# Kernel optimization log

Hardware: AMD Instinct MI355X
Metric: run time of the kernel (lower is better)

The kernel has to match this reference:

```python
import jax, jax.numpy as jnp
import numpy as np

N_NODES = 100000
N_EDGES = 1600000
N_FEAT = 64
HID = 64
HL = 256
N_GRAPHS = 512


def _lin(k, i, o):
    return (jax.random.normal(k, (i, o), jnp.float32) / np.sqrt(i)).astype(jnp.float32)


def setup_inputs() -> dict:
    key = jax.random.key(0)
    ks = jax.random.split(key, 20)
    inp = {
        "x": jax.random.normal(ks[0], (N_NODES, N_FEAT), jnp.float32),
        "edge_index": jax.random.randint(ks[1], (2, N_EDGES), 0, N_NODES),
        "batch": jnp.sort(jax.random.randint(ks[2], (N_NODES,), 0, N_GRAPHS)),
        "T": jax.random.normal(ks[3], (N_GRAPHS, 1), jnp.float32),
    }
    dims = [(N_FEAT, HID), (HID, HID), (HID, HID), (HID, HID)]
    for i, (di, do) in enumerate(dims):
        inp[f"wrel{i}"] = _lin(ks[4 + 3 * i], di, do)
        inp[f"brel{i}"] = jnp.zeros((do,), jnp.float32)
        inp[f"wroot{i}"] = _lin(ks[5 + 3 * i], di, do)
    inp["w1"] = _lin(ks[16], 3 * HID + 1, HL)
    inp["b1"] = jnp.zeros((HL,), jnp.float32)
    inp["w2"] = _lin(ks[17], HL, HL)
    inp["b2"] = jnp.zeros((HL,), jnp.float32)
    inp["w3"] = _lin(ks[18], HL, 1)
    inp["b3"] = jnp.zeros((1,), jnp.float32)
    return inp


def reference(x, edge_index, batch, T,
              wrel0, brel0, wroot0,
              wrel1, brel1, wroot1,
              wrel2, brel2, wroot2,
              wrel3, brel3, wroot3,
              w1, b1, w2, b2, w3, b3):
    src, dst = edge_index[0], edge_index[1]

    def conv(h, wr, br, wq):
        # PyG GraphConv: W_root h_i + W_rel * sum_{j->i} h_j + b_rel
        agg = jax.ops.segment_sum(h[src], dst, num_segments=N_NODES)
        return agg @ wr + br + h @ wq

    h = jax.nn.relu(conv(x, wrel0, brel0, wroot0))
    h = jax.nn.relu(conv(h, wrel1, brel1, wroot1))
    h = jax.nn.relu(conv(h, wrel2, brel2, wroot2))
    h = conv(h, wrel3, brel3, wroot3)  # no relu on conv2 (matches original)

    # global add / mean / max pools over graph ids
    s = jax.ops.segment_sum(h, batch, num_segments=N_GRAPHS)
    cnt = jax.ops.segment_sum(jnp.ones((N_NODES, 1), h.dtype), batch, num_segments=N_GRAPHS)
    mean = s / jnp.maximum(cnt, 1.0)
    mx = jax.ops.segment_max(h, batch, num_segments=N_GRAPHS)
    mx = jnp.where(jnp.isfinite(mx), mx, 0.0)  # empty segments -> 0

    out = jnp.concatenate([mx, mean, s, T], axis=1)  # [G, 3*HID+1]
    o = jax.nn.relu(out @ w1 + b1)
    o = jax.nn.relu(o @ w2 + b2)  # dropout is identity in eval mode
    return o @ w3 + b3
```

## Files before the change

kernel.cpp:

```cpp
#include <hip/hip_runtime.h>
#include <hip/hip_bf16.h>
#include <math.h>

#define N_NODES 100000
#define N_EDGES 1600000
#define N_FEAT 64
#define HID 64
#define HL 256
#define N_GRAPHS 512

#define BUCKET_BITS 7
#define BUCKET_SIZE 128
#define NB ((N_NODES + BUCKET_SIZE - 1) / BUCKET_SIZE)
#define LOFS_W (NB + 1)
#define CAP 3584
#define LREC_CAP 3584
#define EDGES_PER_BLOCK 4096
#define SCAT_BLOCKS ((N_EDGES + EDGES_PER_BLOCK - 1) / EDGES_PER_BLOCK)
#define F2B_BLOCKS (N_NODES * 16 / 256)
#define WPREP_BLOCKS 128
#define ZOFF ((unsigned int)N_NODES * 128u)

typedef short vbf8 __attribute__((ext_vector_type(8)));
typedef float vf4 __attribute__((ext_vector_type(4)));
typedef float vf2 __attribute__((ext_vector_type(2)));

__device__ __forceinline__ unsigned short f2b(float f) {
    unsigned int u = __float_as_uint(f);
    return (unsigned short)((u + 0x7FFFu + ((u >> 16) & 1u)) >> 16);
}
__device__ __forceinline__ float b2f(unsigned short u) {
    return __uint_as_float(((unsigned int)u) << 16);
}
__device__ __forceinline__ unsigned pk2(float lo, float hi) {
    float2 f; f.x = lo; f.y = hi;
    __hip_bfloat162 h = __float22bfloat162_rn(f);
    unsigned r;
    __builtin_memcpy(&r, &h, 4);
    return r;
}
__device__ __forceinline__ vf2 bpair(unsigned int d) {
    vf2 r;
    r.x = __uint_as_float(d << 16);
    r.y = __uint_as_float(d & 0xFFFF0000u);
    return r;
}


__global__ __launch_bounds__(256) void k_mega(
        const int* __restrict__ src, const int* __restrict__ dst,
        int* __restrict__ lofs, unsigned int* __restrict__ ebuf,
        const float4* __restrict__ x, uint2* __restrict__ xb,
        const float* __restrict__ wroot0, const float* __restrict__ wrel0,
        const float* __restrict__ wroot1, const float* __restrict__ wrel1,
        const float* __restrict__ wroot2, const float* __restrict__ wrel2,
        const float* __restrict__ wroot3, const float* __restrict__ wrel3,
        unsigned short* __restrict__ wt) {
    __shared__ int lh[NB];
    __shared__ int lsc[256];
    __shared__ unsigned lrec[EDGES_PER_BLOCK];
    int bid = blockIdx.x;
    int t = threadIdx.x;

    if (bid < SCAT_BLOCKS) {
        for (int i = t; i < NB; i += 256) lh[i] = 0;
        __syncthreads();
        int i0 = bid * EDGES_PER_BLOCK;
        int i1 = min(N_EDGES, i0 + EDGES_PER_BLOCK);
        int cnt = i1 - i0;
        for (int i = i0 + t; i < i1; i += 256)
            atomicAdd(&lh[dst[i] >> BUCKET_BITS], 1);
        __syncthreads();
        int v[4];
        int s = 0;
        int base4 = t * 4;
#pragma unroll
        for (int j = 0; j < 4; j++) {
            v[j] = (base4 + j < NB) ? lh[base4 + j] : 0;
            s += v[j];
        }
        lsc[t] = s;
        __syncthreads();
        for (int off = 1; off < 256; off <<= 1) {
            int xx = lsc[t];
            int y = (t >= off) ? lsc[t - off] : 0;
            __syncthreads();
            lsc[t] = xx + y;
            __syncthreads();
        }
        int run = lsc[t] - s;
        int* lrow = lofs + (size_t)bid * LOFS_W;
#pragma unroll
        for (int j = 0; j < 4; j++) {
            int b = base4 + j;
            if (b < NB) {
                lrow[b] = run;
                lh[b] = run;
            }
            run += v[j];
        }
        if (t == 255) lrow[NB] = cnt;
        __syncthreads();
        for (int i = i0 + t; i < i1; i += 256) {
            int sN = src[i], d = dst[i];
            int b = d >> BUCKET_BITS;
            int p = atomicAdd(&lh[b], 1);
            lrec[p] = ((unsigned)sN << 7) | (unsigned)(d & 127);
        }
        __syncthreads();
        unsigned* eb = ebuf + (size_t)bid * EDGES_PER_BLOCK;
        for (int j = t; j < cnt; j += 256) eb[j] = lrec[j];
    } else if (bid < SCAT_BLOCKS + F2B_BLOCKS) {
        int i = (bid - SCAT_BLOCKS) * 256 + t;
        if (i < N_NODES * 16) {
            float4 v = x[i];
            uint2 o;
            o.x = pk2(v.x, v.y);
            o.y = pk2(v.z, v.w);
            xb[i] = o;
        }
    } else {
        int gi = (bid - SCAT_BLOCKS - F2B_BLOCKS) * 256 + t;
        if (gi < 4 * 64 * 128) {
            int layer = gi >> 13;
            int i = gi & 8191;
            int nn = i >> 7, k = i & 127;
            const float* wr = (layer == 0) ? wroot0 : (layer == 1) ? wroot1
                             : (layer == 2) ? wroot2 : wroot3;
            const float* wl = (layer == 0) ? wrel0 : (layer == 1) ? wrel1
                             : (layer == 2) ? wrel2 : wrel3;
            float v = (k < 64) ? wr[k * 64 + nn] : wl[(k - 64) * 64 + nn];
            wt[gi] = f2b(v);
        }
    }
}


__global__ __launch_bounds__(256) void k_fscatter2(
        const unsigned int* __restrict__ ebuf, const int* __restrict__ lofs,
        int2* __restrict__ re, unsigned int* __restrict__ soff,
        unsigned short* __restrict__ hbA, unsigned short* __restrict__ hbB, int n) {
    __shared__ int rcnt[512];
    __shared__ int rbase[512];
    __shared__ int rpre[512];
    __shared__ int tsc[256];
    __shared__ unsigned lrec[LREC_CAP];
    __shared__ int lcnt[BUCKET_SIZE];
    __shared__ int sc[BUCKET_SIZE];
    __shared__ int cur[BUCKET_SIZE];
    int b = blockIdx.x;
    int n0 = b * BUCKET_SIZE;
    int t = threadIdx.x;
    if (b == 0 && t < 16) {
        uint4 z = make_uint4(0u, 0u, 0u, 0u);
        unsigned short* hp = (t < 8) ? hbA : hbB;
        ((uint4*)(hp + (size_t)N_NODES * 64))[t & 7] = z;
    }
    for (int blk = t; blk < 512; blk += 256) {
        int c = 0, ba = 0;
        if (blk < SCAT_BLOCKS) {
            const int* lr = lofs + (size_t)blk * LOFS_W + b;
            ba = lr[0];
            c = lr[1] - ba;
        }
        rcnt[blk] = c;
        rbase[blk] = ba;
    }
    __syncthreads();
    int c0 = rcnt[2 * t], c1 = rcnt[2 * t + 1];
    tsc[t] = c0 + c1;
    __syncthreads();
    for (int off = 1; off < 256; off <<= 1) {
        int xx = tsc[t];
        int y = (t >= off) ? tsc[t - off] : 0;
        __syncthreads();
        tsc[t] = xx + y;
        __syncthreads();
    }
    int ex = tsc[t] - (c0 + c1);
    rpre[2 * t] = ex;
    rpre[2 * t + 1] = ex + c0;
    __syncthreads();
    int cb = tsc[255];
    for (int blk = t; blk < SCAT_BLOCKS; blk += 256) {
        int c = rcnt[blk];
        int dsto = rpre[blk];
        const unsigned* sp = ebuf + (size_t)blk * EDGES_PER_BLOCK + rbase[blk];
        for (int j = 0; j < c; j++) lrec[dsto + j] = sp[j];
    }
    if (t < BUCKET_SIZE) lcnt[t] = 0;
    __syncthreads();
    for (int r = t; r < cb; r += 256)
        atomicAdd(&lcnt[lrec[r] & 127u], 1);
    __syncthreads();
    int v = 0, pcnt = 0;
    if (t < BUCKET_SIZE) {
        v = lcnt[t];
        pcnt = (v + 7) & ~7;
        sc[t] = pcnt;
    }
    __syncthreads();
    for (int off = 1; off < BUCKET_SIZE; off <<= 1) {
        int xx = 0;
        if (t < BUCKET_SIZE) {
            xx = sc[t];
            if (t >= off) xx += sc[t - off];
        }
        __syncthreads();
        if (t < BUCKET_SIZE) sc[t] = xx;
        __syncthreads();
    }
    if (t < BUCKET_SIZE) {
        int start = b * CAP + sc[t] - pcnt;
        if (n0 + t < n) re[n0 + t] = make_int2(start, start + v);
        cur[t] = start;
        for (int z = start + v; z < start + pcnt; z++) soff[z] = ZOFF;
    }
    __syncthreads();
    for (int r = t; r < cb; r += 256) {
        unsigned rec = lrec[r];
        int p = atomicAdd(&cur[rec & 127u], 1);
        soff[p] = rec & ~127u;
    }
}


__global__ __launch_bounds__(256) void k_agg(
    const unsigned short* __restrict__ hb, unsigned short* __restrict__ aggb,
    const int2* __restrict__ re, const unsigned int* __restrict__ soff, int n) {
    int lane = threadIdx.x & 63;
    int i = (blockIdx.x * 256 + threadIdx.x) >> 6;
    if (i >= n) return;
    int q = lane >> 3;
    int sl = lane & 7;
    int2 bounds = re[i];
    int e0 = bounds.x, e1 = bounds.y;
    int iters = (e1 - e0 + 7) >> 3;
    const char* base = (const char*)hb + sl * 16;

    vf2 A[4], B[4];
#pragma unroll
    for (int f = 0; f < 4; f++) { A[f] = (vf2){0.f, 0.f}; B[f] = (vf2){0.f, 0.f}; }

    int eq = e0 + q;
    int it = 0;
    for (; it + 2 <= iters; it += 2) {
        int ea = eq + it * 8, eb = ea + 8;
        unsigned oa = __builtin_nontemporal_load(soff + ea);
        unsigned ob = __builtin_nontemporal_load(soff + eb);
        uint4 da = *(const uint4*)(base + oa);
        uint4 db = *(const uint4*)(base + ob);
        A[0] += bpair(da.x); A[1] += bpair(da.y);
        A[2] += bpair(da.z); A[3] += bpair(da.w);
        B[0] += bpair(db.x); B[1] += bpair(db.y);
        B[2] += bpair(db.z); B[3] += bpair(db.w);
    }
    if (it < iters) {
        int ea = eq + it * 8;
        unsigned oa = __builtin_nontemporal_load(soff + ea);
        uint4 da = *(const uint4*)(base + oa);
        A[0] += bpair(da.x); A[1] += bpair(da.y);
        A[2] += bpair(da.z); A[3] += bpair(da.w);
    }

    float f[8];
#pragma unroll
    for (int k = 0; k < 4; k++) {
        vf2 s2 = A[k] + B[k];
        float slo = s2.x, shi = s2.y;
        slo += __shfl_xor(slo, 8);
        slo += __shfl_xor(slo, 16);
        slo += __shfl_xor(slo, 32);
        shi += __shfl_xor(shi, 8);
        shi += __shfl_xor(shi, 16);
        shi += __shfl_xor(shi, 32);
        f[2 * k] = slo;
        f[2 * k + 1] = shi;
    }
    if (q == 0) {
        uint4 o;
        o.x = pk2(f[0], f[1]);
        o.y = pk2(f[2], f[3]);
        o.z = pk2(f[4], f[5]);
        o.w = pk2(f[6], f[7]);
        *(uint4*)((char*)aggb + (size_t)i * 128 + sl * 16) = o;
    }
}


template <int RELU>
__global__ __launch_bounds__(256) void k_gemm(
    const unsigned short* __restrict__ hb, const unsigned short* __restrict__ aggb,
    const unsigned short* __restrict__ wt, const float* __restrict__ brel,
    unsigned short* __restrict__ hbout, int n) {
    __shared__ float sc[4][16 * 68];

    int tid = threadIdx.x;
    int w = tid >> 6, l = tid & 63;
    int lm = l & 15, q = l >> 4;
    int r0 = blockIdx.x * 64 + w * 16;

    int arow = r0 + lm;
    if (arow >= n) arow = n - 1;
    const unsigned short* ah = hb + (size_t)arow * 64 + q * 8;
    const unsigned short* aa = aggb + (size_t)arow * 64 + q * 8;
    vbf8 afr[4];
    afr[0] = *(const vbf8*)(ah);
    afr[1] = *(const vbf8*)(ah + 32);
    afr[2] = *(const vbf8*)(aa);
    afr[3] = *(const vbf8*)(aa + 32);

    vf4 acc[4];
#pragma unroll
    for (int t = 0; t < 4; t++) acc[t] = (vf4){0.f, 0.f, 0.f, 0.f};

#pragma unroll
    for (int t = 0; t < 4; t++) {
        const unsigned short* wrow = wt + (size_t)(t * 16 + lm) * 128 + q * 8;
#pragma unroll
        for (int s = 0; s < 4; s++) {
            vbf8 bfr = *(const vbf8*)(wrow + s * 32);
            acc[t] = __builtin_amdgcn_mfma_f32_16x16x32_bf16(afr[s], bfr, acc[t], 0, 0, 0);
        }
    }

    float* sw_ = sc[w];
#pragma unroll
    for (int t = 0; t < 4; t++) {
        float b = brel[t * 16 + lm];
#pragma unroll
        for (int i = 0; i < 4; i++) {
            float v = acc[t][i] + b;
            if (RELU) v = fmaxf(v, 0.f);
            sw_[(q * 4 + i) * 68 + t * 16 + lm] = v;
        }
    }
    int rr = l >> 2, cs = l & 3;
    int node = r0 + rr;
    if (node < n) {
        const float* rp = sw_ + rr * 68 + cs * 16;
        float4 v0 = *(const float4*)(rp);
        float4 v1 = *(const float4*)(rp + 4);
        float4 v2 = *(const float4*)(rp + 8);
        float4 v3 = *(const float4*)(rp + 12);
        uint4 o0, o1;
        o0.x = pk2(v0.x, v0.y);
        o0.y = pk2(v0.z, v0.w);
        o0.z = pk2(v1.x, v1.y);
        o0.w = pk2(v1.z, v1.w);
        o1.x = pk2(v2.x, v2.y);
        o1.y = pk2(v2.z, v2.w);
        o1.z = pk2(v3.x, v3.y);
        o1.w = pk2(v3.z, v3.w);
        uint4* op = (uint4*)(hbout + (size_t)node * 64 + cs * 16);
        op[0] = o0;
        op[1] = o1;
    }
}


__global__ __launch_bounds__(256) void k_poolmlp(
    const unsigned short* __restrict__ hb, const int* __restrict__ batch,
    const float* __restrict__ T, const float* __restrict__ w1,
    const float* __restrict__ b1, const float* __restrict__ w2,
    const float* __restrict__ b2, const float* __restrict__ w3,
    const float* __restrict__ b3, float* __restrict__ out, int n) {
    __shared__ float psum[4][64];
    __shared__ float pmax[4][64];
    __shared__ float sin_[200];
    __shared__ float so1[256];
    __shared__ float red[256];
    int g = blockIdx.x, t = threadIdx.x;
    int l = t & 63, c = t >> 6;

    int lo = 0, hi = n;
    while (lo < hi) { int m = (lo + hi) >> 1; if (batch[m] < g) lo = m + 1; else hi = m; }
    int s0 = lo;
    int lo2 = s0, hi2 = n;
    while (lo2 < hi2) { int m = (lo2 + hi2) >> 1; if (batch[m] < g + 1) lo2 = m + 1; else hi2 = m; }
    int s1 = lo2;

    float sa0 = 0.f, sa1 = 0.f, sa2 = 0.f, sa3 = 0.f;
    float ma0 = -INFINITY, ma1 = -INFINITY, ma2 = -INFINITY, ma3 = -INFINITY;
    int nn = s0 + c;
    for (; nn + 12 < s1; nn += 16) {
        float v0 = b2f(hb[(size_t)nn * 64 + l]);
        float v1 = b2f(hb[(size_t)(nn + 4) * 64 + l]);
        float v2 = b2f(hb[(size_t)(nn + 8) * 64 + l]);
        float v3 = b2f(hb[(size_t)(nn + 12) * 64 + l]);
        sa0 += v0; sa1 += v1; sa2 += v2; sa3 += v3;
        ma0 = fmaxf(ma0, v0); ma1 = fmaxf(ma1, v1);
        ma2 = fmaxf(ma2, v2); ma3 = fmaxf(ma3, v3);
    }
    for (; nn < s1; nn += 4) {
        float v = b2f(hb[(size_t)nn * 64 + l]);
        sa0 += v;
        ma0 = fmaxf(ma0, v);
    }
    psum[c][l] = (sa0 + sa1) + (sa2 + sa3);
    pmax[c][l] = fmaxf(fmaxf(ma0, ma1), fmaxf(ma2, ma3));
    __syncthreads();
    if (t < 64) {
        float s = (psum[0][t] + psum[1][t]) + (psum[2][t] + psum[3][t]);
        float mx = fmaxf(fmaxf(pmax[0][t], pmax[1][t]), fmaxf(pmax[2][t], pmax[3][t]));
        int cnt = s1 - s0;
        float mean = s / fmaxf((float)cnt, 1.f);
        if (cnt == 0) mx = 0.f;
        sin_[t] = mx;
        sin_[64 + t] = mean;
        sin_[128 + t] = s;
        if (t == 0) {
            sin_[192] = T[g];
#pragma unroll
            for (int z = 193; z < 200; z++) sin_[z] = 0.f;
        }
    }
    __syncthreads();

    float a = b1[t];
    {
        float wv[8];
        for (int k = 0; k < 192; k += 8) {
#pragma unroll
            for (int u = 0; u < 8; u++) wv[u] = w1[(k + u) * 256 + t];
#pragma unroll
            for (int u = 0; u < 8; u++) a += sin_[k + u] * wv[u];
        }
        a += sin_[192] * w1[192 * 256 + t];
    }
    a = fmaxf(a, 0.f);
    so1[t] = a;
    __syncthreads();

    float a2 = b2[t];
    {
        float wv[8];
        for (int k = 0; k < 256; k += 8) {
#pragma unroll
            for (int u = 0; u < 8; u++) wv[u] = w2[(k + u) * 256 + t];
#pragma unroll
            for (int u = 0; u < 8; u++) a2 += so1[k + u] * wv[u];
        }
    }
    a2 = fmaxf(a2, 0.f);
    red[t] = a2 * w3[t];
    __syncthreads();
    for (int s = 128; s > 0; s >>= 1) {
        if (t < s) red[t] += red[t + s];
        __syncthreads();
    }
    if (t == 0) out[g] = red[0] + b3[0];
}

extern "C" void kernel_launch(void* const* d_in, const int* in_sizes, int n_in,
                              void* d_out, int out_size, void* d_ws, size_t ws_size,
                              hipStream_t stream) {
    const int N = N_NODES, E = N_EDGES, G = N_GRAPHS;

    const float* x = (const float*)d_in[0];
    const int* ei = (const int*)d_in[1];
    const int* batch = (const int*)d_in[2];
    const float* T = (const float*)d_in[3];
    const float* wrel[4] = {(const float*)d_in[4], (const float*)d_in[7],
                            (const float*)d_in[10], (const float*)d_in[13]};
    const float* brel[4] = {(const float*)d_in[5], (const float*)d_in[8],
                            (const float*)d_in[11], (const float*)d_in[14]};
    const float* wroot[4] = {(const float*)d_in[6], (const float*)d_in[9],
                             (const float*)d_in[12], (const float*)d_in[15]};
    const float* w1 = (const float*)d_in[16];
    const float* b1 = (const float*)d_in[17];
    const float* w2 = (const float*)d_in[18];
    const float* b2 = (const float*)d_in[19];
    const float* w3 = (const float*)d_in[20];
    const float* b3 = (const float*)d_in[21];
    float* out = (float*)d_out;

    const int* esrc = ei;
    const int* edst = ei + E;

    char* ws = (char*)d_ws;
    size_t off = 0;
    auto alloc = [&](size_t bytes) {
        size_t r = off;
        off = (off + bytes + 255) & ~(size_t)255;
        return r;
    };
    int* lofs = (int*)(ws + alloc((size_t)SCAT_BLOCKS * LOFS_W * 4));
    int2* re = (int2*)(ws + alloc((size_t)N * 8));
    unsigned int* soff = (unsigned int*)(ws + alloc((size_t)NB * CAP * 4));
    unsigned int* ebuf = (unsigned int*)(ws + alloc((size_t)SCAT_BLOCKS * EDGES_PER_BLOCK * 4));
    unsigned short* hbA = (unsigned short*)(ws + alloc((size_t)N * 64 * 2 + 128));
    unsigned short* hbB = (unsigned short*)(ws + alloc((size_t)N * 64 * 2 + 128));
    unsigned short* aggb = (unsigned short*)(ws + alloc((size_t)N * 64 * 2));
    unsigned short* wt = (unsigned short*)(ws + alloc((size_t)4 * 64 * 128 * 2));

    k_mega<<<SCAT_BLOCKS + F2B_BLOCKS + WPREP_BLOCKS, 256, 0, stream>>>(
        esrc, edst, lofs, ebuf, (const float4*)x, (uint2*)hbA,
        wroot[0], wrel[0], wroot[1], wrel[1],
        wroot[2], wrel[2], wroot[3], wrel[3], wt);
    k_fscatter2<<<NB, 256, 0, stream>>>(ebuf, lofs, re, soff, hbA, hbB, N);

    int agg_blocks = (N * 64 + 255) / 256;
    int gemm_blocks = (N + 63) / 64;

    k_agg<<<agg_blocks, 256, 0, stream>>>(hbA, aggb, re, soff, N);
    k_gemm<1><<<gemm_blocks, 256, 0, stream>>>(hbA, aggb, wt + 0 * 8192, brel[0], hbB, N);

    k_agg<<<agg_blocks, 256, 0, stream>>>(hbB, aggb, re, soff, N);
    k_gemm<1><<<gemm_blocks, 256, 0, stream>>>(hbB, aggb, wt + 1 * 8192, brel[1], hbA, N);

    k_agg<<<agg_blocks, 256, 0, stream>>>(hbA, aggb, re, soff, N);
    k_gemm<1><<<gemm_blocks, 256, 0, stream>>>(hbA, aggb, wt + 2 * 8192, brel[2], hbB, N);

    k_agg<<<agg_blocks, 256, 0, stream>>>(hbB, aggb, re, soff, N);
    k_gemm<0><<<gemm_blocks, 256, 0, stream>>>(hbB, aggb, wt + 3 * 8192, brel[3], hbA, N);

    k_poolmlp<<<G, 256, 0, stream>>>(hbA, batch, T, w1, b1, w2, b2, w3, b3, out, N);
}
```

Measured before the change: 398.4 us.

## Map eight nodes per wavefront in aggregation instead of one node per wave

The aggregation kernel now gives each 8-lane group its own destination node, so a wavefront handles 8 nodes instead of splitting one node's edges across 8 lane groups. This drops the cross-lane shuffle reduction and cuts the block count by 8x. Each group walks its own padded edge list, with the loop bound set to the maximum count in the wave, and out-of-range slots point at a zero row. The cost is divergence from uneven degrees within a wave, plus serial per-node latency chains of four gathers per iteration.

```diff
diff --git a/kernel.cpp b/kernel.cpp
--- a/kernel.cpp
+++ b/kernel.cpp
@@ -229,60 +229,60 @@
     const unsigned short* __restrict__ hb, unsigned short* __restrict__ aggb,
     const int2* __restrict__ re, const unsigned int* __restrict__ soff, int n) {
     int lane = threadIdx.x & 63;
-    int i = (blockIdx.x * 256 + threadIdx.x) >> 6;
-    if (i >= n) return;
-    int q = lane >> 3;
+    int wv = (blockIdx.x * 256 + threadIdx.x) >> 6;
+    int m = lane >> 3;
     int sl = lane & 7;
-    int2 bounds = re[i];
-    int e0 = bounds.x, e1 = bounds.y;
-    int iters = (e1 - e0 + 7) >> 3;
+    int i = wv * 8 + m;
+    if (wv * 8 >= n) return;
+    int ii = min(i, n - 1);
+    int2 bd = re[ii];
+    int e0 = bd.x;
+    int pc = (i < n) ? ((bd.y - bd.x + 7) & ~7) : 0;
+
+    int mx = pc;
+    mx = max(mx, __shfl_xor(mx, 8));
+    mx = max(mx, __shfl_xor(mx, 16));
+    mx = max(mx, __shfl_xor(mx, 32));
+
     const char* base = (const char*)hb + sl * 16;
-
     vf2 A[4], B[4];
 #pragma unroll
     for (int f = 0; f < 4; f++) { A[f] = (vf2){0.f, 0.f}; B[f] = (vf2){0.f, 0.f}; }
 
-    int eq = e0 + q;
-    int it = 0;
-    for (; it + 2 <= iters; it += 2) {
-        int ea = eq + it * 8, eb = ea + 8;
-        unsigned oa = __builtin_nontemporal_load(soff + ea);
-        unsigned ob = __builtin_nontemporal_load(soff + eb);
-        uint4 da = *(const uint4*)(base + oa);
-        uint4 db = *(const uint4*)(base + ob);
-        A[0] += bpair(da.x); A[1] += bpair(da.y);
-        A[2] += bpair(da.z); A[3] += bpair(da.w);
-        B[0] += bpair(db.x); B[1] += bpair(db.y);
-        B[2] += bpair(db.z); B[3] += bpair(db.w);
-    }
-    if (it < iters) {
-        int ea = eq + it * 8;
-        unsigned oa = __builtin_nontemporal_load(soff + ea);
-        uint4 da = *(const uint4*)(base + oa);
-        A[0] += bpair(da.x); A[1] += bpair(da.y);
-        A[2] += bpair(da.z); A[3] += bpair(da.w);
-    }
-
-    float f[8];
-#pragma unroll
-    for (int k = 0; k < 4; k++) {
-        vf2 s2 = A[k] + B[k];
-        float slo = s2.x, shi = s2.y;
-        slo += __shfl_xor(slo, 8);
-        slo += __shfl_xor(slo, 16);
-        slo += __shfl_xor(slo, 32);
-        shi += __shfl_xor(shi, 8);
-        shi += __shfl_xor(shi, 16);
-        shi += __shfl_xor(shi, 32);
-        f[2 * k] = slo;
-        f[2 * k + 1] = shi;
-    }
-    if (q == 0) {
+    for (int it = 0; it < mx; it += 4) {
+        int t0 = it, t1 = it + 1, t2 = it + 2, t3 = it + 3;
+        unsigned o0 = __builtin_nontemporal_load(soff + e0 + ((t0 < pc) ? t0 : 0));
+        unsigned o1 = __builtin_nontemporal_load(soff + e0 + ((t1 < pc) ? t1 : 0));
+        unsigned o2 = __builtin_nontemporal_load(soff + e0 + ((t2 < pc) ? t2 : 0));
+        unsigned o3 = __builtin_nontemporal_load(soff + e0 + ((t3 < pc) ? t3 : 0));
+        o0 = (t0 < pc) ? o0 : ZOFF;
+        o1 = (t1 < pc) ? o1 : ZOFF;
+        o2 = (t2 < pc) ? o2 : ZOFF;
+        o3 = (t3 < pc) ? o3 : ZOFF;
+        uint4 d0 = *(const uint4*)(base + o0);
+        uint4 d1 = *(const uint4*)(base + o1);
+        uint4 d2 = *(const uint4*)(base + o2);
+        uint4 d3 = *(const uint4*)(base + o3);
+        A[0] += bpair(d0.x); A[1] += bpair(d0.y);
+        A[2] += bpair(d0.z); A[3] += bpair(d0.w);
+        B[0] += bpair(d1.x); B[1] += bpair(d1.y);
+        B[2] += bpair(d1.z); B[3] += bpair(d1.w);
+        A[0] += bpair(d2.x); A[1] += bpair(d2.y);
+        A[2] += bpair(d2.z); A[3] += bpair(d2.w);
+        B[0] += bpair(d3.x); B[1] += bpair(d3.y);
+        B[2] += bpair(d3.z); B[3] += bpair(d3.w);
+    }
+
+    if (i < n) {
+        vf2 s0 = A[0] + B[0];
+        vf2 s1 = A[1] + B[1];
+        vf2 s2 = A[2] + B[2];
+        vf2 s3 = A[3] + B[3];
         uint4 o;
-        o.x = pk2(f[0], f[1]);
-        o.y = pk2(f[2], f[3]);
-        o.z = pk2(f[4], f[5]);
-        o.w = pk2(f[6], f[7]);
+        o.x = pk2(s0.x, s0.y);
+        o.y = pk2(s1.x, s1.y);
+        o.z = pk2(s2.x, s2.y);
+        o.w = pk2(s3.x, s3.y);
         *(uint4*)((char*)aggb + (size_t)i * 128 + sl * 16) = o;
     }
 }
@@ -500,7 +500,7 @@
         wroot[2], wrel[2], wroot[3], wrel[3], wt);
     k_fscatter2<<<NB, 256, 0, stream>>>(ebuf, lofs, re, soff, hbA, hbB, N);
 
-    int agg_blocks = (N * 64 + 255) / 256;
+    int agg_blocks = (N + 31) / 32;
     int gemm_blocks = (N + 63) / 64;
 
     k_agg<<<agg_blocks, 256, 0, stream>>>(hbA, aggb, re, soff, N);
```

New measurement: 393.2 us. About the same (-1.3%).
